# Kernel tuning notes

Hardware: AMD Instinct MI355X
Metric: run time of the kernel (lower is better)

Reference implementation:

```python
import jax, jax.numpy as jnp
import numpy as np

BN_EPS = 1e-5


def setup_inputs() -> dict:
    key = jax.random.key(0)
    ks = jax.random.split(key, 6)
    N, F, H, C, E = 50000, 128, 256, 40, 800000
    x = jax.random.normal(ks[0], (N, F), dtype=jnp.float32)
    edge_index = jax.random.randint(ks[1], (2, E), 0, N, dtype=jnp.int64)
    eps = jnp.zeros((), dtype=jnp.float32)  # train_eps=True, init 0
    W1 = jax.random.normal(ks[2], (F, H), dtype=jnp.float32) * (1.0 / np.sqrt(F))
    b1 = jnp.zeros((H,), dtype=jnp.float32)
    gamma = jnp.ones((H,), dtype=jnp.float32)
    beta = jnp.zeros((H,), dtype=jnp.float32)
    W2 = jax.random.normal(ks[3], (H, C), dtype=jnp.float32) * (1.0 / np.sqrt(H))
    b2 = jnp.zeros((C,), dtype=jnp.float32)
    return {"x": x, "edge_index": edge_index, "eps": eps, "W1": W1, "b1": b1,
            "gamma": gamma, "beta": beta, "W2": W2, "b2": b2}


def reference(x, edge_index, eps, W1, b1, gamma, beta, W2, b2):
    N = x.shape[0]
    src, dst = edge_index[0], edge_index[1]  # source_to_target flow
    # GIN sum aggregation: sum_{j in N(i)} x_j  (scatter-add over edges)
    agg = jax.ops.segment_sum(x[src], dst, num_segments=N)
    h = (1.0 + eps) * x + agg  # [N, F]
    # MLP: Linear -> ReLU (act_first) -> BatchNorm -> Linear (plain last)
    h = jax.nn.relu(h @ W1 + b1)  # [N, H]
    mean = jnp.mean(h, axis=0)
    var = jnp.var(h, axis=0)  # biased var, training-mode batch norm
    h = (h - mean) * jax.lax.rsqrt(var + BN_EPS) * gamma + beta
    out = h @ W2 + b2  # [N, C]
    return jax.nn.log_softmax(out, axis=-1)
```

## Files before the change

### kernel.cpp

```cpp
#include <hip/hip_runtime.h>
#include <hip/hip_bf16.h>
#include <math.h>

#define F_IN 128
#define H_DIM 256
#define C_OUT 40

typedef __attribute__((ext_vector_type(8))) short short8v;
typedef __attribute__((ext_vector_type(4))) float float4v;

__device__ __forceinline__ unsigned short f2bf(float f) {
    union { float f; unsigned int u; } c; c.f = f;
    unsigned int r = (c.u + 0x7fffu + ((c.u >> 16) & 1u)) >> 16;
    return (unsigned short)r;
}
__device__ __forceinline__ float bf2f(unsigned short u) {
    union { unsigned int u; float f; } c; c.u = ((unsigned int)u) << 16;
    return c.f;
}

__global__ __launch_bounds__(256) void prep(const float* __restrict__ x,
                                            const float* __restrict__ W1,
                                            unsigned short* __restrict__ x_b,
                                            unsigned short* __restrict__ w1t,
                                            int* __restrict__ head,
                                            int N, int nA) {
    int b = blockIdx.x;
    if (b < nA) {
        long long i = ((long long)b * 256 + threadIdx.x) * 8;
        if (i + 7 < (long long)N * F_IN) {
            float4 v0 = *reinterpret_cast<const float4*>(x + i);
            float4 v1 = *reinterpret_cast<const float4*>(x + i + 4);
            short8v o;
            o[0] = (short)f2bf(v0.x); o[1] = (short)f2bf(v0.y);
            o[2] = (short)f2bf(v0.z); o[3] = (short)f2bf(v0.w);
            o[4] = (short)f2bf(v1.x); o[5] = (short)f2bf(v1.y);
            o[6] = (short)f2bf(v1.z); o[7] = (short)f2bf(v1.w);
            *reinterpret_cast<short8v*>(x_b + i) = o;
        }
    } else if (b < nA + 128) {
        int t = (b - nA) * 2 + (threadIdx.x >> 7);
        int k = threadIdx.x & 127;
        w1t[t * F_IN + k] = f2bf(W1[(size_t)k * H_DIM + t]);
    } else {
        int i = (b - nA - 128) * 256 + threadIdx.x;
        if (i < N) head[i] = -1;
    }
}

__global__ __launch_bounds__(256) void build_list(const int* __restrict__ src,
                                                  const int* __restrict__ dst,
                                                  int* __restrict__ head,
                                                  int2* __restrict__ listbuf, int E) {
    int i = blockIdx.x * 256 + threadIdx.x;
    if (i >= E) return;
    int d = dst[i];
    int prev = atomicExch(&head[d], i);
    listbuf[i] = make_int2(src[i], prev);
}

__global__ __launch_bounds__(256) void gather_agg(const unsigned short* __restrict__ xb,
                                                  const float* __restrict__ epsp,
                                                  const int* __restrict__ head,
                                                  const int2* __restrict__ listbuf,
                                                  unsigned short* __restrict__ aggb, int N) {
    int wave = (blockIdx.x * 256 + (int)threadIdx.x) >> 6;
    int lane = threadIdx.x & 63;
    int g = lane >> 3;
    int lr = lane & 7;
    int node = wave * 8 + g;
    bool valid = node < N;
    int j = valid ? head[node] : -1;

    float acc[16] = {};
    while (__any(j >= 0)) {
        if (j >= 0) {
            int2 e = listbuf[j];
            const unsigned short* rp = xb + (size_t)e.x * F_IN + lr * 16;
            short8v v0 = *reinterpret_cast<const short8v*>(rp);
            short8v v1 = *reinterpret_cast<const short8v*>(rp + 8);
            j = e.y;
            #pragma unroll
            for (int t = 0; t < 8; ++t) acc[t] += bf2f((unsigned short)v0[t]);
            #pragma unroll
            for (int t = 0; t < 8; ++t) acc[8 + t] += bf2f((unsigned short)v1[t]);
        }
    }

    if (valid) {
        float sc = 1.0f + epsp[0];
        const unsigned short* xp = xb + (size_t)node * F_IN + lr * 16;
        short8v x0 = *reinterpret_cast<const short8v*>(xp);
        short8v x1 = *reinterpret_cast<const short8v*>(xp + 8);
        short8v o0, o1;
        #pragma unroll
        for (int t = 0; t < 8; ++t) {
            o0[t] = (short)f2bf(fmaf(sc, bf2f((unsigned short)x0[t]), acc[t]));
            o1[t] = (short)f2bf(fmaf(sc, bf2f((unsigned short)x1[t]), acc[8 + t]));
        }
        unsigned short* op = aggb + (size_t)node * F_IN + lr * 16;
        *reinterpret_cast<short8v*>(op) = o0;
        *reinterpret_cast<short8v*>(op + 8) = o1;
    }
}

__global__ __launch_bounds__(256) void gemm1_mfma(const unsigned short* __restrict__ agg_b,
                                                  const unsigned short* __restrict__ w1t,
                                                  const float* __restrict__ b1,
                                                  unsigned short* __restrict__ h1,
                                                  float* __restrict__ partials, int N) {
    __shared__ short As[128][136];
    __shared__ short Bs[64][136];
    __shared__ float sums_l[64], ssq_l[64];

    int tid = threadIdx.x;
    int m0 = blockIdx.x * 128;
    int n0 = blockIdx.y * 64;

    if (tid < 64) { sums_l[tid] = 0.f; ssq_l[tid] = 0.f; }

    #pragma unroll
    for (int i = 0; i < 8; ++i) {
        int c = tid + i * 256;
        int row = c >> 4, ck = c & 15;
        int gr = m0 + row;
        short8v v = {0, 0, 0, 0, 0, 0, 0, 0};
        if (gr < N) v = *reinterpret_cast<const short8v*>(agg_b + (size_t)gr * F_IN + ck * 8);
        *reinterpret_cast<short8v*>(&As[row][ck * 8]) = v;
    }
    #pragma unroll
    for (int i = 0; i < 4; ++i) {
        int c = tid + i * 256;
        int row = c >> 4, ck = c & 15;
        *reinterpret_cast<short8v*>(&Bs[row][ck * 8]) =
            *reinterpret_cast<const short8v*>(w1t + (size_t)(n0 + row) * F_IN + ck * 8);
    }
    __syncthreads();

    int w = tid >> 6, lane = tid & 63;
    int wm = w >> 1, wn = w & 1;
    int lr = lane & 15, lk = (lane >> 4) * 8;

    float4v acc[4][2] = {};
    #pragma unroll
    for (int ks = 0; ks < 4; ++ks) {
        int k0 = ks * 32 + lk;
        short8v a[4], b[2];
        #pragma unroll
        for (int am = 0; am < 4; ++am)
            a[am] = *reinterpret_cast<short8v*>(&As[wm * 64 + am * 16 + lr][k0]);
        #pragma unroll
        for (int bn = 0; bn < 2; ++bn)
            b[bn] = *reinterpret_cast<short8v*>(&Bs[wn * 32 + bn * 16 + lr][k0]);
        #pragma unroll
        for (int am = 0; am < 4; ++am)
            #pragma unroll
            for (int bn = 0; bn < 2; ++bn)
                acc[am][bn] = __builtin_amdgcn_mfma_f32_16x16x32_bf16(a[am], b[bn], acc[am][bn], 0, 0, 0);
    }

    __syncthreads();
    short (*T)[72] = reinterpret_cast<short (*)[72]>(&As[0][0]);
    #pragma unroll
    for (int bn = 0; bn < 2; ++bn) {
        int col = wn * 32 + bn * 16 + lr;
        float bias = b1[n0 + col];
        float ps = 0.f, pss = 0.f;
        #pragma unroll
        for (int am = 0; am < 4; ++am) {
            #pragma unroll
            for (int r = 0; r < 4; ++r) {
                int rowl = wm * 64 + am * 16 + (lane >> 4) * 4 + r;
                float v = fmaxf(acc[am][bn][r] + bias, 0.f);
                unsigned short ub = f2bf(v);
                T[rowl][col] = (short)ub;
                if (m0 + rowl < N) {
                    float vr = bf2f(ub);
                    ps += vr;
                    pss = fmaf(vr, vr, pss);
                }
            }
        }
        atomicAdd(&sums_l[col], ps);
        atomicAdd(&ssq_l[col], pss);
    }
    __syncthreads();

    #pragma unroll
    for (int i = 0; i < 4; ++i) {
        int c = tid + i * 256;
        int row = c >> 3, ck = c & 7;
        int gr = m0 + row;
        if (gr < N)
            *reinterpret_cast<short8v*>(h1 + (size_t)gr * H_DIM + n0 + ck * 8) =
                *reinterpret_cast<short8v*>(&T[row][ck * 8]);
    }
    if (tid < 64) {
        size_t base = (size_t)blockIdx.x * 512;
        partials[base + n0 + tid] = sums_l[tid];
        partials[base + 256 + n0 + tid] = ssq_l[tid];
    }
}

__global__ __launch_bounds__(256) void bn_reduce(const float* __restrict__ partials,
                                                 int nbx,
                                                 float* __restrict__ sums,
                                                 float* __restrict__ sumsq) {
    __shared__ float red[8];
    int k = blockIdx.x;
    float s = 0.f, ss = 0.f;
    for (int b = threadIdx.x; b < nbx; b += 256) {
        s += partials[(size_t)b * 512 + k];
        ss += partials[(size_t)b * 512 + 256 + k];
    }
    #pragma unroll
    for (int off = 32; off > 0; off >>= 1) {
        s += __shfl_down(s, off, 64);
        ss += __shfl_down(ss, off, 64);
    }
    int wave = threadIdx.x >> 6;
    int lane = threadIdx.x & 63;
    if (lane == 0) { red[wave] = s; red[4 + wave] = ss; }
    __syncthreads();
    if (threadIdx.x == 0) {
        sums[k] = red[0] + red[1] + red[2] + red[3];
        sumsq[k] = red[4] + red[5] + red[6] + red[7];
    }
}

__global__ __launch_bounds__(256) void bn_fold(const float* __restrict__ sums,
                                               const float* __restrict__ sumsq,
                                               const float* __restrict__ gamma,
                                               const float* __restrict__ beta,
                                               const float* __restrict__ W2,
                                               const float* __restrict__ b2,
                                               unsigned short* __restrict__ w2frag,
                                               float* __restrict__ b2f, int N) {
    __shared__ float scale_s[H_DIM], shift_s[H_DIM];
    int k = threadIdx.x;
    float invN = 1.0f / (float)N;
    float mean = sums[k] * invN;
    float var = sumsq[k] * invN - mean * mean;
    float scale = gamma[k] * rsqrtf(var + 1e-5f);
    float shift = beta[k] - mean * scale;
    scale_s[k] = scale;
    shift_s[k] = shift;
    __syncthreads();
    if (k < 48) {
        if (k < C_OUT) {
            float acc = b2[k];
            for (int j = 0; j < H_DIM; ++j) acc = fmaf(shift_s[j], W2[j * C_OUT + k], acc);
            b2f[k] = acc;
        } else {
            b2f[k] = -1e30f;
        }
    }
    for (int u = threadIdx.x; u < 1536; u += 256) {
        int lane = u & 63, t = u >> 6;
        int ks = t / 3, bf = t - ks * 3;
        int col = bf * 16 + (lane & 15);
        int kb = ks * 32 + (lane >> 4) * 8;
        short8v o;
        #pragma unroll
        for (int e = 0; e < 8; ++e) {
            int kk = kb + e;
            float v = (col < C_OUT) ? scale_s[kk] * W2[kk * C_OUT + col] : 0.f;
            o[e] = (short)f2bf(v);
        }
        *reinterpret_cast<short8v*>(w2frag + (size_t)u * 8) = o;
    }
}

__global__ __launch_bounds__(256) void gemm2_lsm(const unsigned short* __restrict__ h1,
                                                 const unsigned short* __restrict__ w2frag,
                                                 const float* __restrict__ b2f,
                                                 float* __restrict__ out, int N) {
    int tid = threadIdx.x;
    int wm = tid >> 6;
    int lane = tid & 63;
    int lr = lane & 15;
    int g = lane >> 4;
    int row0 = blockIdx.x * 64 + wm * 16;
    int arow = row0 + lr;
    if (arow >= N) arow = N - 1;

    short8v a[8];
    const unsigned short* ap = h1 + (size_t)arow * H_DIM + g * 8;
    #pragma unroll
    for (int ks = 0; ks < 8; ++ks)
        a[ks] = *reinterpret_cast<const short8v*>(ap + ks * 32);

    float4v acc[3] = {};
    #pragma unroll
    for (int ks = 0; ks < 8; ++ks) {
        #pragma unroll
        for (int bf = 0; bf < 3; ++bf) {
            short8v b = *reinterpret_cast<const short8v*>(
                w2frag + (size_t)(((ks * 3 + bf) << 6) + lane) * 8);
            acc[bf] = __builtin_amdgcn_mfma_f32_16x16x32_bf16(a[ks], b, acc[bf], 0, 0, 0);
        }
    }

    float b0 = b2f[lr], b1v = b2f[16 + lr], b2v = b2f[32 + lr];
    #pragma unroll
    for (int r = 0; r < 4; ++r) {
        float v0 = acc[0][r] + b0;
        float v1 = acc[1][r] + b1v;
        float v2 = acc[2][r] + b2v;
        float m = fmaxf(fmaxf(v0, v1), v2);
        #pragma unroll
        for (int o = 1; o < 16; o <<= 1) m = fmaxf(m, __shfl_xor(m, o, 64));
        float s = __expf(v0 - m) + __expf(v1 - m) + __expf(v2 - m);
        #pragma unroll
        for (int o = 1; o < 16; o <<= 1) s += __shfl_xor(s, o, 64);
        float lse = m + __logf(s);
        int row = row0 + g * 4 + r;
        if (row < N) {
            float* op = out + (size_t)row * C_OUT;
            op[lr] = v0 - lse;
            op[16 + lr] = v1 - lse;
            if (lr < 8) op[32 + lr] = v2 - lse;
        }
    }
}

extern "C" void kernel_launch(void* const* d_in, const int* in_sizes, int n_in,
                              void* d_out, int out_size, void* d_ws, size_t ws_size,
                              hipStream_t stream) {
    const float* x     = (const float*)d_in[0];
    const int*   ei    = (const int*)d_in[1];
    const float* eps   = (const float*)d_in[2];
    const float* W1    = (const float*)d_in[3];
    const float* b1    = (const float*)d_in[4];
    const float* gamma = (const float*)d_in[5];
    const float* beta  = (const float*)d_in[6];
    const float* W2    = (const float*)d_in[7];
    const float* b2    = (const float*)d_in[8];
    float* out = (float*)d_out;

    int N = in_sizes[0] / F_IN;
    int E = in_sizes[1] / 2;
    const int* srcIdx = ei;
    const int* dstIdx = ei + E;

    int nbx = (N + 127) / 128;

    unsigned short* x_b    = (unsigned short*)d_ws;
    unsigned short* agg_b  = x_b + (size_t)N * F_IN;
    unsigned short* w1t    = agg_b + (size_t)N * F_IN;
    unsigned short* h1     = w1t + H_DIM * F_IN;
    float* partials = (float*)(h1 + (size_t)N * H_DIM);
    float* sums   = partials + (size_t)nbx * 512;
    float* sumsq  = sums + H_DIM;
    unsigned short* w2frag = (unsigned short*)(sumsq + H_DIM);
    float* b2f    = (float*)(w2frag + 1536 * 8);

    int*  head    = (int*)h1;
    int2* listbuf = (int2*)(head + N);

    int nA = (N * 16 + 255) / 256;
    int nZ = (N + 255) / 256;
    hipLaunchKernelGGL(prep, dim3(nA + 128 + nZ), dim3(256), 0, stream,
                       x, W1, x_b, w1t, head, N, nA);

    hipLaunchKernelGGL(build_list, dim3((E + 255) / 256), dim3(256), 0, stream,
                       srcIdx, dstIdx, head, listbuf, E);

    hipLaunchKernelGGL(gather_agg, dim3((N + 31) / 32), dim3(256), 0, stream,
                       x_b, eps, head, listbuf, agg_b, N);

    dim3 g1(nbx, H_DIM / 64);
    hipLaunchKernelGGL(gemm1_mfma, g1, dim3(256), 0, stream,
                       agg_b, w1t, b1, h1, partials, N);

    hipLaunchKernelGGL(bn_reduce, dim3(H_DIM), dim3(256), 0, stream,
                       partials, nbx, sums, sumsq);

    hipLaunchKernelGGL(bn_fold, dim3(1), dim3(H_DIM), 0, stream,
                       sums, sumsq, gamma, beta, W2, b2, w2frag, b2f, N);

    hipLaunchKernelGGL(gemm2_lsm, dim3((N + 63) / 64), dim3(256), 0, stream,
                       h1, w2frag, b2f, out, N);
}
```

Before: 149.2 us.

## Fuse edge-list build into prep kernel and widen GEMM1 N-tile to 128

```diff
diff --git a/kernel.cpp b/kernel.cpp
--- a/kernel.cpp
+++ b/kernel.cpp
@@ -21,10 +21,13 @@
 
 __global__ __launch_bounds__(256) void prep(const float* __restrict__ x,
                                             const float* __restrict__ W1,
+                                            const int* __restrict__ src,
+                                            const int* __restrict__ dst,
                                             unsigned short* __restrict__ x_b,
                                             unsigned short* __restrict__ w1t,
                                             int* __restrict__ head,
-                                            int N, int nA) {
+                                            int2* __restrict__ listbuf,
+                                            int N, int E, int nA) {
     int b = blockIdx.x;
     if (b < nA) {
         long long i = ((long long)b * 256 + threadIdx.x) * 8;
@@ -44,19 +47,12 @@
         w1t[t * F_IN + k] = f2bf(W1[(size_t)k * H_DIM + t]);
     } else {
         int i = (b - nA - 128) * 256 + threadIdx.x;
-        if (i < N) head[i] = -1;
-    }
-}
-
-__global__ __launch_bounds__(256) void build_list(const int* __restrict__ src,
-                                                  const int* __restrict__ dst,
-                                                  int* __restrict__ head,
-                                                  int2* __restrict__ listbuf, int E) {
-    int i = blockIdx.x * 256 + threadIdx.x;
-    if (i >= E) return;
-    int d = dst[i];
-    int prev = atomicExch(&head[d], i);
-    listbuf[i] = make_int2(src[i], prev);
+        if (i < E) {
+            int d = dst[i];
+            int prev = atomicExch(&head[d], i + 1);
+            listbuf[i] = make_int2(src[i], prev);
+        }
+    }
 }
 
 __global__ __launch_bounds__(256) void gather_agg(const unsigned short* __restrict__ xb,
@@ -70,12 +66,12 @@
     int lr = lane & 7;
     int node = wave * 8 + g;
     bool valid = node < N;
-    int j = valid ? head[node] : -1;
+    int j = valid ? head[node] : 0;
 
     float acc[16] = {};
-    while (__any(j >= 0)) {
-        if (j >= 0) {
-            int2 e = listbuf[j];
+    while (__any(j > 0)) {
+        if (j > 0) {
+            int2 e = listbuf[j - 1];
             const unsigned short* rp = xb + (size_t)e.x * F_IN + lr * 16;
             short8v v0 = *reinterpret_cast<const short8v*>(rp);
             short8v v1 = *reinterpret_cast<const short8v*>(rp + 8);
@@ -110,14 +106,14 @@
                                                   unsigned short* __restrict__ h1,
                                                   float* __restrict__ partials, int N) {
     __shared__ short As[128][136];
-    __shared__ short Bs[64][136];
-    __shared__ float sums_l[64], ssq_l[64];
+    __shared__ short Bs[128][136];
+    __shared__ float sums_l[128], ssq_l[128];
 
     int tid = threadIdx.x;
     int m0 = blockIdx.x * 128;
-    int n0 = blockIdx.y * 64;
-
-    if (tid < 64) { sums_l[tid] = 0.f; ssq_l[tid] = 0.f; }
+    int n0 = blockIdx.y * 128;
+
+    if (tid < 128) { sums_l[tid] = 0.f; ssq_l[tid] = 0.f; }
 
     #pragma unroll
     for (int i = 0; i < 8; ++i) {
@@ -129,7 +125,7 @@
         *reinterpret_cast<short8v*>(&As[row][ck * 8]) = v;
     }
     #pragma unroll
-    for (int i = 0; i < 4; ++i) {
+    for (int i = 0; i < 8; ++i) {
         int c = tid + i * 256;
         int row = c >> 4, ck = c & 15;
         *reinterpret_cast<short8v*>(&Bs[row][ck * 8]) =
@@ -141,29 +137,29 @@
     int wm = w >> 1, wn = w & 1;
     int lr = lane & 15, lk = (lane >> 4) * 8;
 
-    float4v acc[4][2] = {};
+    float4v acc[4][4] = {};
     #pragma unroll
     for (int ks = 0; ks < 4; ++ks) {
         int k0 = ks * 32 + lk;
-        short8v a[4], b[2];
+        short8v a[4], b[4];
         #pragma unroll
         for (int am = 0; am < 4; ++am)
             a[am] = *reinterpret_cast<short8v*>(&As[wm * 64 + am * 16 + lr][k0]);
         #pragma unroll
-        for (int bn = 0; bn < 2; ++bn)
-            b[bn] = *reinterpret_cast<short8v*>(&Bs[wn * 32 + bn * 16 + lr][k0]);
+        for (int bn = 0; bn < 4; ++bn)
+            b[bn] = *reinterpret_cast<short8v*>(&Bs[wn * 64 + bn * 16 + lr][k0]);
         #pragma unroll
         for (int am = 0; am < 4; ++am)
             #pragma unroll
-            for (int bn = 0; bn < 2; ++bn)
+            for (int bn = 0; bn < 4; ++bn)
                 acc[am][bn] = __builtin_amdgcn_mfma_f32_16x16x32_bf16(a[am], b[bn], acc[am][bn], 0, 0, 0);
     }
 
     __syncthreads();
-    short (*T)[72] = reinterpret_cast<short (*)[72]>(&As[0][0]);
-    #pragma unroll
-    for (int bn = 0; bn < 2; ++bn) {
-        int col = wn * 32 + bn * 16 + lr;
+    short (*T)[136] = As;
+    #pragma unroll
+    for (int bn = 0; bn < 4; ++bn) {
+        int col = wn * 64 + bn * 16 + lr;
         float bias = b1[n0 + col];
         float ps = 0.f, pss = 0.f;
         #pragma unroll
@@ -187,15 +183,15 @@
     __syncthreads();
 
     #pragma unroll
-    for (int i = 0; i < 4; ++i) {
+    for (int i = 0; i < 8; ++i) {
         int c = tid + i * 256;
-        int row = c >> 3, ck = c & 7;
+        int row = c >> 4, ck = c & 15;
         int gr = m0 + row;
         if (gr < N)
             *reinterpret_cast<short8v*>(h1 + (size_t)gr * H_DIM + n0 + ck * 8) =
                 *reinterpret_cast<short8v*>(&T[row][ck * 8]);
     }
-    if (tid < 64) {
+    if (tid < 128) {
         size_t base = (size_t)blockIdx.x * 512;
         partials[base + n0 + tid] = sums_l[tid];
         partials[base + 256 + n0 + tid] = ssq_l[tid];
@@ -358,18 +354,17 @@
     int*  head    = (int*)h1;
     int2* listbuf = (int2*)(head + N);
 
+    hipMemsetAsync(head, 0, (size_t)N * sizeof(int), stream);
+
     int nA = (N * 16 + 255) / 256;
-    int nZ = (N + 255) / 256;
-    hipLaunchKernelGGL(prep, dim3(nA + 128 + nZ), dim3(256), 0, stream,
-                       x, W1, x_b, w1t, head, N, nA);
-
-    hipLaunchKernelGGL(build_list, dim3((E + 255) / 256), dim3(256), 0, stream,
-                       srcIdx, dstIdx, head, listbuf, E);
+    int nE = (E + 255) / 256;
+    hipLaunchKernelGGL(prep, dim3(nA + 128 + nE), dim3(256), 0, stream,
+                       x, W1, srcIdx, dstIdx, x_b, w1t, head, listbuf, N, E, nA);
 
     hipLaunchKernelGGL(gather_agg, dim3((N + 31) / 32), dim3(256), 0, stream,
                        x_b, eps, head, listbuf, agg_b, N);
 
-    dim3 g1(nbx, H_DIM / 64);
+    dim3 g1(nbx, 2);
     hipLaunchKernelGGL(gemm1_mfma, g1, dim3(256), 0, stream,
                        agg_b, w1t, b1, h1, partials, N);
 
```

New measurement: 161.5 us. 8.2% more time.
